# Performance work log

Measured on AMD Instinct MI355X. Metric: run time of the kernel, lower is better.

Reference implementation:

```python
import jax, jax.numpy as jnp
import numpy as np

N = 100000   # nodes
E = 1600000  # edges
D = 128      # input_dim == hidden_dim
G = 64       # graphs in batch
EPS = 1e-5


def setup_inputs() -> dict:
    key = jax.random.key(0)
    ks = jax.random.split(key, 16)
    s = 1.0 / np.sqrt(D)
    inp = {
        "x": jax.random.normal(ks[0], (N, D), jnp.float32),
        "edge_index": jax.random.randint(ks[1], (2, E), 0, N, jnp.int64),
        "batch": jnp.sort(jax.random.randint(ks[2], (N,), 0, G, jnp.int64)),
        # 4 blocks x 2 SAGEConv layers = 8 convs, all DxD
        "Wl": jax.random.normal(ks[3], (8, D, D), jnp.float32) * s,
        "bl": jnp.zeros((8, D), jnp.float32),
        "Wr": jax.random.normal(ks[4], (8, D, D), jnp.float32) * s,
        "gamma": jnp.ones((4, D), jnp.float32),
        "beta": jnp.zeros((4, D), jnp.float32),
        # classifier: 2D -> D -> D//2 -> 1
        "W1": jax.random.normal(ks[5], (2 * D, D), jnp.float32) / np.sqrt(2 * D),
        "b1": jnp.zeros((D,), jnp.float32),
        "W2": jax.random.normal(ks[6], (D, D // 2), jnp.float32) * s,
        "b2": jnp.zeros((D // 2,), jnp.float32),
        "W3": jax.random.normal(ks[7], (D // 2, 1), jnp.float32) / np.sqrt(D // 2),
        "b3": jnp.zeros((1,), jnp.float32),
    }
    return inp


def _sage_conv(h, src, dst, inv_deg, W_l, b_l, W_r):
    # mean-aggregate neighbor features (messages flow src -> dst)
    agg = jax.ops.segment_sum(h[src], dst, num_segments=N) * inv_deg
    return agg @ W_l + b_l + h @ W_r


def _forward(x, edge_index, batch, Wl, bl, Wr, gamma, beta, W1, b1, W2, b2, W3, b3):
    src, dst = edge_index[0], edge_index[1]
    deg = jax.ops.segment_sum(jnp.ones((E,), x.dtype), dst, num_segments=N)
    inv_deg = (1.0 / jnp.maximum(deg, 1.0))[:, None]  # [N,1]

    h = x
    for blk in range(4):
        # GraphSAGE(in, hid, num_layers=2): conv -> relu -> conv
        h = _sage_conv(h, src, dst, inv_deg, Wl[2 * blk], bl[2 * blk], Wr[2 * blk])
        h = jax.nn.relu(h)
        h = _sage_conv(h, src, dst, inv_deg, Wl[2 * blk + 1], bl[2 * blk + 1], Wr[2 * blk + 1])
        # BatchNorm1d over nodes (training-mode batch statistics, biased var)
        mu = jnp.mean(h, axis=0)
        var = jnp.var(h, axis=0)
        h = (h - mu) * jax.lax.rsqrt(var + EPS) * gamma[blk] + beta[blk]
        h = jax.nn.relu(h)  # dropout is identity in eval mode

    # global mean / max pool over graph ids
    cnt = jax.ops.segment_sum(jnp.ones((N,), h.dtype), batch, num_segments=G)
    x_mean = jax.ops.segment_sum(h, batch, num_segments=G) / jnp.maximum(cnt, 1.0)[:, None]
    x_max = jax.ops.segment_max(h, batch, num_segments=G)
    g = jnp.concatenate([x_mean, x_max], axis=1)  # [G, 2D]

    g = jax.nn.relu(g @ W1 + b1)
    g = jax.nn.relu(g @ W2 + b2)
    return g @ W3 + b3  # [G, 1]


def reference(x, edge_index, batch, Wl, bl, Wr, gamma, beta, W1, b1, W2, b2, W3, b3):
    return _forward(x, edge_index, batch, Wl, bl, Wr, gamma, beta, W1, b1, W2, b2, W3, b3)
```

## Files before the change

### kernel.cpp

```cpp
#include <hip/hip_runtime.h>
#include <hip/hip_bf16.h>
#include <math.h>

#define NN 100000
#define NE 1600000
#define DIM 128
#define NG 64
#define EPSBN 1e-5f
#define NGB 1563
#define SORT_WIN 12500
#define NBINBLK 6250
#define DSL 64

typedef unsigned int u32;
typedef unsigned short u16;
typedef __attribute__((ext_vector_type(8))) short bf8_t;
typedef __attribute__((ext_vector_type(4))) float f4_t;
typedef __attribute__((ext_vector_type(4))) unsigned short u16x4;
#define MFMA(a, b, c) __builtin_amdgcn_mfma_f32_16x16x32_bf16((a), (b), (c), 0, 0, 0)

__device__ __forceinline__ u16 f2bf(float f) {
    u32 u = __float_as_uint(f);
    u32 r = u + 0x7FFFu + ((u >> 16) & 1u);
    return (u16)(r >> 16);
}
__device__ __forceinline__ float bf2f(u16 h) { return __uint_as_float(((u32)h) << 16); }

__global__ void k_bin_cnt(const int* __restrict__ ei, int* __restrict__ blkcnt) {
    __shared__ int c[8];
    int t = threadIdx.x;
    if (t < 8) c[t] = 0;
    __syncthreads();
    int e = blockIdx.x * 256 + t;
    int d = ei[NE + e];
    atomicAdd(&c[d / SORT_WIN], 1);
    __syncthreads();
    if (t < 8) blkcnt[blockIdx.x * 8 + t] = c[t];
}

__global__ void k_bin_scan(const int* __restrict__ blkcnt, int* __restrict__ blkoff,
                           int* __restrict__ wtotal) {
    __shared__ int ps[256];
    int w = blockIdx.x, t = threadIdx.x;
    const int PER = (NBINBLK + 255) / 256;
    int s = 0;
    for (int i = 0; i < PER; ++i) {
        int b = t * PER + i;
        if (b < NBINBLK) s += blkcnt[b * 8 + w];
    }
    ps[t] = s;
    for (int off = 1; off < 256; off <<= 1) {
        __syncthreads();
        int x = (t >= off) ? ps[t - off] : 0;
        __syncthreads();
        ps[t] += x;
    }
    __syncthreads();
    int run = (t ? ps[t - 1] : 0);
    for (int i = 0; i < PER; ++i) {
        int b = t * PER + i;
        if (b < NBINBLK) { blkoff[b * 8 + w] = run; run += blkcnt[b * 8 + w]; }
    }
    if (t == 255) wtotal[w] = ps[255];
}

__global__ void k_bin_start(const int* __restrict__ wtotal, int* __restrict__ binStart) {
    if (threadIdx.x == 0) {
        int a = 0;
        for (int w = 0; w < 8; ++w) { binStart[w] = a; a += wtotal[w]; }
        binStart[8] = a;
    }
}

__global__ void k_bin_place(const int* __restrict__ ei, const int* __restrict__ blkoff,
                            const int* __restrict__ binStart, int2* __restrict__ binned) {
    __shared__ int base[8];
    int t = threadIdx.x;
    if (t < 8) base[t] = binStart[t] + blkoff[blockIdx.x * 8 + t];
    __syncthreads();
    int e = blockIdx.x * 256 + t;
    int s = ei[e], d = ei[NE + e];
    int pos = atomicAdd(&base[d / SORT_WIN], 1);
    binned[pos] = make_int2(s, d);
}

__global__ void k_deg2(const int2* __restrict__ binned, const int* __restrict__ binStart,
                       int* __restrict__ deg) {
    int w = blockIdx.x & 7, sl = blockIdx.x >> 3;
    int b0 = binStart[w], b1 = binStart[w + 1];
    int chunk = (b1 - b0 + DSL - 1) / DSL;
    int r0 = b0 + sl * chunk, r1 = min(r0 + chunk, b1);
    for (int i = r0 + threadIdx.x; i < r1; i += 256)
        atomicAdd(&deg[binned[i].y], 1);
}

__global__ void k_scatter(const int2* __restrict__ binned, const int* __restrict__ binStart,
                          int* __restrict__ cursor, int* __restrict__ sorted_src) {
    int w = blockIdx.x & 7, sl = blockIdx.x >> 3;
    int b0 = binStart[w], b1 = binStart[w + 1];
    int chunk = (b1 - b0 + DSL - 1) / DSL;
    int r0 = b0 + sl * chunk, r1 = min(r0 + chunk, b1);
    for (int i = r0 + threadIdx.x; i < r1; i += 256) {
        int2 e = binned[i];
        int pos = atomicAdd(&cursor[e.y], 1);
        sorted_src[pos] = e.x;
    }
}

#define SCAN_B 256
__global__ void k_scan1(const int* __restrict__ deg, int* __restrict__ row_start,
                        int* __restrict__ bsum, float* __restrict__ inv_deg) {
    __shared__ int s[SCAN_B];
    int t = threadIdx.x;
    int i = blockIdx.x * SCAN_B + t;
    int v = (i < NN) ? deg[i] : 0;
    if (i < NN) inv_deg[i] = 1.0f / (float)(v > 1 ? v : 1);
    s[t] = v;
    for (int off = 1; off < SCAN_B; off <<= 1) {
        __syncthreads();
        int x = (t >= off) ? s[t - off] : 0;
        __syncthreads();
        s[t] += x;
    }
    if (i < NN) row_start[i + 1] = s[t];
    if (t == SCAN_B - 1) bsum[blockIdx.x] = s[t];
}

__global__ void k_scan2(int* __restrict__ bsum, int nb) {
    __shared__ int s[512];
    int t = threadIdx.x;
    int v = (t < nb) ? bsum[t] : 0;
    s[t] = v;
    for (int off = 1; off < 512; off <<= 1) {
        __syncthreads();
        int x = (t >= off) ? s[t - off] : 0;
        __syncthreads();
        s[t] += x;
    }
    if (t < nb) bsum[t] = s[t] - v;
}

__global__ void k_scan3(int* __restrict__ row_start, const int* __restrict__ bsum,
                        int* __restrict__ cursor) {
    int i = blockIdx.x * blockDim.x + threadIdx.x;
    if (i < NN) {
        int v = row_start[i + 1] + bsum[i / SCAN_B];
        row_start[i + 1] = v;
        if (i + 1 < NN) cursor[i + 1] = v;
    }
    if (i == 0) { row_start[0] = 0; cursor[0] = 0; }
}

__global__ void k_bounds(const int* __restrict__ batch, int* __restrict__ gs) {
    int g = threadIdx.x;
    if (g > NG) return;
    int lo = 0, hi = NN;
    while (lo < hi) {
        int mid = (lo + hi) >> 1;
        if (batch[mid] < g) lo = mid + 1; else hi = mid;
    }
    gs[g] = lo;
}

__global__ void k_split_x(const float* __restrict__ x, u16* __restrict__ Xh,
                          u16* __restrict__ Xl) {
    int idx = blockIdx.x * 256 + threadIdx.x;
    int base = idx * 4;
    float4 v = *reinterpret_cast<const float4*>(&x[base]);
    u16x4 hi, lo;
    float vv[4] = {v.x, v.y, v.z, v.w};
#pragma unroll
    for (int j = 0; j < 4; j++) {
        u16 h = f2bf(vv[j]);
        hi[j] = h;
        lo[j] = f2bf(vv[j] - bf2f(h));
    }
    *reinterpret_cast<u16x4*>(&Xh[base]) = hi;
    *reinterpret_cast<u16x4*>(&Xl[base]) = lo;
}

__global__ void k_prep_w(const float* __restrict__ Wl, const float* __restrict__ Wr,
                         u16* __restrict__ Wth, u16* __restrict__ Wtl) {
    int idx = blockIdx.x * 256 + threadIdx.x;
    int k = idx & 255;
    int col = (idx >> 8) & 127;
    int c = idx >> 15;
    float v = (k < 128) ? Wl[(c * 128 + k) * 128 + col] : Wr[(c * 128 + (k - 128)) * 128 + col];
    u16 h = f2bf(v);
    Wth[idx] = h;
    Wtl[idx] = f2bf(v - bf2f(h));
}

template <int AFF>
__global__ void k_aggregate(const u16* __restrict__ Hh,
                            const int* __restrict__ row_start, const int* __restrict__ ssrc,
                            const float* __restrict__ inv_deg, const float* __restrict__ ss,
                            u16* __restrict__ Ah, u16* __restrict__ Al) {
    int wid = blockIdx.x * 4 + (threadIdx.x >> 6);
    int lane = threadIdx.x & 63;
    int half = lane >> 5;
    int cl = lane & 31;
    if (wid >= NN) return;
    float sc0 = 0.f, sc1 = 0.f, sc2 = 0.f, sc3 = 0.f;
    float sh0 = 0.f, sh1 = 0.f, sh2 = 0.f, sh3 = 0.f;
    if (AFF) {
        float4 s4 = *reinterpret_cast<const float4*>(ss + cl * 4);
        float4 h4 = *reinterpret_cast<const float4*>(ss + 128 + cl * 4);
        sc0 = s4.x; sc1 = s4.y; sc2 = s4.z; sc3 = s4.w;
        sh0 = h4.x; sh1 = h4.y; sh2 = h4.z; sh3 = h4.w;
    }
    int beg = row_start[wid], end = row_start[wid + 1];
    int n = end - beg;
    float a0 = 0.f, a1 = 0.f, a2 = 0.f, a3 = 0.f;
#define ACCUM(vv)                                                                   \
    {                                                                               \
        float t0 = __uint_as_float((vv).x << 16);                                   \
        float t1 = __uint_as_float((vv).x & 0xFFFF0000u);                           \
        float t2 = __uint_as_float((vv).y << 16);                                   \
        float t3 = __uint_as_float((vv).y & 0xFFFF0000u);                           \
        if (AFF) {                                                                  \
            t0 = fmaxf(t0 * sc0 + sh0, 0.f); t1 = fmaxf(t1 * sc1 + sh1, 0.f);       \
            t2 = fmaxf(t2 * sc2 + sh2, 0.f); t3 = fmaxf(t3 * sc3 + sh3, 0.f);       \
        }                                                                           \
        a0 += t0; a1 += t1; a2 += t2; a3 += t3;                                     \
    }
    for (int base = 0; base < n; base += 64) {
        int rem = n - base;
        int idx = beg + base + (lane < rem ? lane : 0);
        int sv = ssrc[idx];
        int m = rem < 64 ? rem : 64;
        int j = 0;
        for (; j + 4 <= m; j += 4) {
            int sA = __shfl(sv, j + half);
            int sB = __shfl(sv, j + 2 + half);
            uint2 vA = *reinterpret_cast<const uint2*>(
                reinterpret_cast<const u32*>(Hh + (size_t)sA * DIM) + cl * 2);
            uint2 vB = *reinterpret_cast<const uint2*>(
                reinterpret_cast<const u32*>(Hh + (size_t)sB * DIM) + cl * 2);
            ACCUM(vA); ACCUM(vB);
        }
        for (; j < m; j += 2) {
            if (j + half < m) {
                int s0 = __shfl(sv, j + half);
                uint2 v = *reinterpret_cast<const uint2*>(
                    reinterpret_cast<const u32*>(Hh + (size_t)s0 * DIM) + cl * 2);
                ACCUM(v);
            }
        }
    }
#undef ACCUM
    a0 += __shfl_down(a0, 32);
    a1 += __shfl_down(a1, 32);
    a2 += __shfl_down(a2, 32);
    a3 += __shfl_down(a3, 32);
    if (half == 0) {
        float sc = inv_deg[wid];
        a0 *= sc; a1 *= sc; a2 *= sc; a3 *= sc;
        u16 h0 = f2bf(a0), h1 = f2bf(a1), h2 = f2bf(a2), h3 = f2bf(a3);
        u16 l0 = f2bf(a0 - bf2f(h0)), l1 = f2bf(a1 - bf2f(h1));
        u16 l2 = f2bf(a2 - bf2f(h2)), l3 = f2bf(a3 - bf2f(h3));
        uint2 hv = make_uint2((u32)h0 | ((u32)h1 << 16), (u32)h2 | ((u32)h3 << 16));
        uint2 lv = make_uint2((u32)l0 | ((u32)l1 << 16), (u32)l2 | ((u32)l3 << 16));
        *reinterpret_cast<uint2*>(Ah + (size_t)wid * DIM + cl * 4) = hv;
        *reinterpret_cast<uint2*>(Al + (size_t)wid * DIM + cl * 4) = lv;
    }
}

__device__ __forceinline__ void affine_split(bf8_t& h, bf8_t& l,
                                             const float* __restrict__ ss, int k0) {
#pragma unroll
    for (int j = 0; j < 8; ++j) {
        float v = bf2f((u16)h[j]) + bf2f((u16)l[j]);
        v = fmaxf(v * ss[k0 + j] + ss[128 + k0 + j], 0.f);
        u16 hh = f2bf(v);
        h[j] = (short)hh;
        l[j] = (short)f2bf(v - bf2f(hh));
    }
}

template <bool RELU, bool STATS, bool AFF2>
__global__ __launch_bounds__(256, 2) void k_gemm(
    const u16* __restrict__ A1h, const u16* __restrict__ A1l,
    const u16* __restrict__ A2h, const u16* __restrict__ A2l,
    const u16* __restrict__ Wth, const u16* __restrict__ Wtl,
    const float* __restrict__ bias, const float* __restrict__ ss,
    u16* __restrict__ Oh, u16* __restrict__ Ol,
    float* __restrict__ partials) {
    __shared__ float cs[128], cq[128];
    int t = threadIdx.x;
    int w = t >> 6, l = t & 63;
    int rl = l & 15, kg = l >> 4;
    int col0 = w * 32;
    int rbase = blockIdx.x * 64;
    int rc0 = min(rbase + rl, NN - 1);
    int rc1 = min(rbase + 16 + rl, NN - 1);
    int rc2 = min(rbase + 32 + rl, NN - 1);
    int rc3 = min(rbase + 48 + rl, NN - 1);

    bf8_t wh[2][8], wlo[2][8];
#pragma unroll
    for (int cf = 0; cf < 2; ++cf) {
        const u16* pw = Wth + (size_t)(col0 + cf * 16 + rl) * 256 + kg * 8;
        const u16* pl = Wtl + (size_t)(col0 + cf * 16 + rl) * 256 + kg * 8;
#pragma unroll
        for (int kc = 0; kc < 8; ++kc) {
            wh[cf][kc] = *reinterpret_cast<const bf8_t*>(pw + kc * 32);
            wlo[cf][kc] = *reinterpret_cast<const bf8_t*>(pl + kc * 32);
        }
    }

    f4_t acc[4][2];
#pragma unroll
    for (int i = 0; i < 4; ++i)
#pragma unroll
        for (int j = 0; j < 2; ++j) acc[i][j] = (f4_t){0.f, 0.f, 0.f, 0.f};

    bf8_t aH[4], aL[4], bH[4], bL[4];

#define LOADK(kc, H, L)                                                          \
    {                                                                            \
        const u16* _bh = ((kc) < 4) ? A1h : A2h;                                 \
        const u16* _bl = ((kc) < 4) ? A1l : A2l;                                 \
        int _ko = ((kc) & 3) * 32 + kg * 8;                                      \
        H[0] = *reinterpret_cast<const bf8_t*>(_bh + (size_t)rc0 * DIM + _ko);   \
        L[0] = *reinterpret_cast<const bf8_t*>(_bl + (size_t)rc0 * DIM + _ko);   \
        H[1] = *reinterpret_cast<const bf8_t*>(_bh + (size_t)rc1 * DIM + _ko);   \
        L[1] = *reinterpret_cast<const bf8_t*>(_bl + (size_t)rc1 * DIM + _ko);   \
        H[2] = *reinterpret_cast<const bf8_t*>(_bh + (size_t)rc2 * DIM + _ko);   \
        L[2] = *reinterpret_cast<const bf8_t*>(_bl + (size_t)rc2 * DIM + _ko);   \
        H[3] = *reinterpret_cast<const bf8_t*>(_bh + (size_t)rc3 * DIM + _ko);   \
        L[3] = *reinterpret_cast<const bf8_t*>(_bl + (size_t)rc3 * DIM + _ko);   \
    }

#define COMPK(kc, H, L)                                                          \
    {                                                                            \
        if (AFF2 && (kc) >= 4) {                                                 \
            int _k0 = ((kc) - 4) * 32 + kg * 8;                                  \
            affine_split(H[0], L[0], ss, _k0);                                   \
            affine_split(H[1], L[1], ss, _k0);                                   \
            affine_split(H[2], L[2], ss, _k0);                                   \
            affine_split(H[3], L[3], ss, _k0);                                   \
        }                                                                        \
        _Pragma("unroll")                                                        \
        for (int _rf = 0; _rf < 4; ++_rf) {                                      \
            _Pragma("unroll")                                                    \
            for (int _cf = 0; _cf < 2; ++_cf) {                                  \
                acc[_rf][_cf] = MFMA(H[_rf], wh[_cf][(kc)], acc[_rf][_cf]);      \
                acc[_rf][_cf] = MFMA(H[_rf], wlo[_cf][(kc)], acc[_rf][_cf]);     \
                acc[_rf][_cf] = MFMA(L[_rf], wh[_cf][(kc)], acc[_rf][_cf]);      \
            }                                                                    \
        }                                                                        \
    }

    LOADK(0, aH, aL)
    LOADK(1, bH, bL) COMPK(0, aH, aL)
    LOADK(2, aH, aL) COMPK(1, bH, bL)
    LOADK(3, bH, bL) COMPK(2, aH, aL)
    LOADK(4, aH, aL) COMPK(3, bH, bL)
    LOADK(5, bH, bL) COMPK(4, aH, aL)
    LOADK(6, aH, aL) COMPK(5, bH, bL)
    LOADK(7, bH, bL) COMPK(6, aH, aL)
    COMPK(7, bH, bL)
#undef LOADK
#undef COMPK

    float bv0 = bias[col0 + rl];
    float bv1 = bias[col0 + 16 + rl];
    float s0 = 0.f, q0 = 0.f, s1 = 0.f, q1 = 0.f;
#pragma unroll
    for (int rf = 0; rf < 4; ++rf) {
#pragma unroll
        for (int i = 0; i < 4; ++i) {
            int row = rbase + rf * 16 + kg * 4 + i;
            if (row < NN) {
                float v = acc[rf][0][i] + bv0;
                if (RELU) v = fmaxf(v, 0.f);
                u16 hi = f2bf(v);
                Oh[(size_t)row * DIM + col0 + rl] = hi;
                Ol[(size_t)row * DIM + col0 + rl] = f2bf(v - bf2f(hi));
                if (STATS) { s0 += v; q0 += v * v; }
                float v1 = acc[rf][1][i] + bv1;
                if (RELU) v1 = fmaxf(v1, 0.f);
                u16 hi1 = f2bf(v1);
                Oh[(size_t)row * DIM + col0 + 16 + rl] = hi1;
                Ol[(size_t)row * DIM + col0 + 16 + rl] = f2bf(v1 - bf2f(hi1));
                if (STATS) { s1 += v1; q1 += v1 * v1; }
            }
        }
    }
    if (STATS) {
        s0 += __shfl_xor(s0, 16); s0 += __shfl_xor(s0, 32);
        q0 += __shfl_xor(q0, 16); q0 += __shfl_xor(q0, 32);
        s1 += __shfl_xor(s1, 16); s1 += __shfl_xor(s1, 32);
        q1 += __shfl_xor(q1, 16); q1 += __shfl_xor(q1, 32);
        if (l < 16) {
            cs[col0 + rl] = s0; cq[col0 + rl] = q0;
            cs[col0 + 16 + rl] = s1; cq[col0 + 16 + rl] = q1;
        }
        __syncthreads();
        partials[(size_t)blockIdx.x * 256 + t] = (t < 128) ? cs[t] : cq[t - 128];
    }
}

__global__ void k_bn_r1(const float* __restrict__ partials, float* __restrict__ colpart) {
    int t = threadIdx.x;
    int b = blockIdx.x;
    int b0 = b * 49, b1 = min(b0 + 49, NGB);
    float s = 0.f;
    for (int i = b0; i < b1; ++i) s += partials[i * 256 + t];
    colpart[b * 256 + t] = s;
}

__global__ void k_bn_r2(const float* __restrict__ colpart, const float* __restrict__ gamma,
                        const float* __restrict__ beta, float* __restrict__ scaleshift) {
    __shared__ float sm[256];
    int t = threadIdx.x;
    float s = 0.f;
#pragma unroll
    for (int b = 0; b < 32; ++b) s += colpart[b * 256 + t];
    sm[t] = s;
    __syncthreads();
    if (t < 128) {
        float mu = sm[t] * (1.0f / NN);
        float var = sm[t + 128] * (1.0f / NN) - mu * mu;
        float sc = rsqrtf(var + EPSBN) * gamma[t];
        scaleshift[t] = sc;
        scaleshift[t + 128] = beta[t] - mu * sc;
    }
}

__global__ void k_pool(const u16* __restrict__ Hh, const int* __restrict__ gs,
                       const float* __restrict__ ss,
                       float* __restrict__ pSum, float* __restrict__ pMax) {
    int g = blockIdx.x >> 3, slice = blockIdx.x & 7;
    int s0 = gs[g], s1 = gs[g + 1];
    int len = s1 - s0;
    int chunk = (len + 7) >> 3;
    int r0 = s0 + slice * chunk;
    int r1 = min(r0 + chunk, s1);
    int t = threadIdx.x;
    int c2 = (t & 63) * 2, half = t >> 6;
    float sc0 = ss[c2], sc1 = ss[c2 + 1];
    float sh0 = ss[128 + c2], sh1 = ss[128 + c2 + 1];
    float sa = 0.f, sb = 0.f, ma = 0.f, mb = 0.f;
    for (int r = r0 + half; r < r1; r += 4) {
        u32 h2 = *reinterpret_cast<const u32*>(Hh + r * DIM + c2);
        float v0 = fmaxf(__uint_as_float(h2 << 16) * sc0 + sh0, 0.f);
        float v1 = fmaxf(__uint_as_float(h2 & 0xFFFF0000u) * sc1 + sh1, 0.f);
        sa += v0; sb += v1;
        ma = fmaxf(ma, v0); mb = fmaxf(mb, v1);
    }
    __shared__ float ls[4][128], lm[4][128];
    ls[half][c2] = sa; ls[half][c2 + 1] = sb;
    lm[half][c2] = ma; lm[half][c2 + 1] = mb;
    __syncthreads();
    if (t < 128) {
        float s = ls[0][t] + ls[1][t] + ls[2][t] + ls[3][t];
        float m = fmaxf(fmaxf(lm[0][t], lm[1][t]), fmaxf(lm[2][t], lm[3][t]));
        atomicAdd(&pSum[g * DIM + t], s);
        atomicMax((int*)&pMax[g * DIM + t], __float_as_int(m));
    }
}

__global__ void k_mlp(const float* __restrict__ pSum, const float* __restrict__ pMax,
                      const int* __restrict__ gs,
                      const float* __restrict__ W1, const float* __restrict__ b1,
                      const float* __restrict__ W2, const float* __restrict__ b2,
                      const float* __restrict__ W3, const float* __restrict__ b3,
                      float* __restrict__ out) {
    __shared__ float g[256], y1[128], y2[64];
    int gi = blockIdx.x;
    int t = threadIdx.x;
    int cnt = gs[gi + 1] - gs[gi];
    float inv = 1.0f / fmaxf((float)cnt, 1.0f);
    g[t] = pSum[gi * DIM + t] * inv;
    g[128 + t] = pMax[gi * DIM + t];
    __syncthreads();
    float a = b1[t];
    for (int k = 0; k < 256; k++) a += g[k] * W1[k * 128 + t];
    y1[t] = fmaxf(a, 0.f);
    __syncthreads();
    if (t < 64) {
        float a2 = b2[t];
        for (int k = 0; k < 128; k++) a2 += y1[k] * W2[k * 64 + t];
        y2[t] = fmaxf(a2, 0.f);
    }
    __syncthreads();
    if (t < 64) {
        float p = y2[t] * W3[t];
#pragma unroll
        for (int off = 32; off; off >>= 1) p += __shfl_down(p, off);
        if (t == 0) out[gi] = p + b3[0];
    }
}

extern "C" void kernel_launch(void* const* d_in, const int* in_sizes, int n_in,
                              void* d_out, int out_size, void* d_ws, size_t ws_size,
                              hipStream_t stream) {
    const float* x     = (const float*)d_in[0];
    const int*   ei    = (const int*)d_in[1];
    const int*   batch = (const int*)d_in[2];
    const float* Wl    = (const float*)d_in[3];
    const float* bl    = (const float*)d_in[4];
    const float* Wr    = (const float*)d_in[5];
    const float* gamma = (const float*)d_in[6];
    const float* beta  = (const float*)d_in[7];
    const float* W1    = (const float*)d_in[8];
    const float* b1    = (const float*)d_in[9];
    const float* W2    = (const float*)d_in[10];
    const float* b2    = (const float*)d_in[11];
    const float* W3    = (const float*)d_in[12];
    const float* b3    = (const float*)d_in[13];
    float* out = (float*)d_out;

    char* p = (char*)d_ws;
    size_t off = 0;
    auto alloc = [&](size_t bytes) -> void* {
        void* r = p + off;
        off += (bytes + 255) & ~(size_t)255;
        return r;
    };
    const size_t HB = (size_t)NN * DIM * 2;
    u16* Xh   = (u16*)alloc(HB);
    u16* Xl   = (u16*)alloc(HB);
    u16* hAh  = (u16*)alloc(HB);
    u16* hAl  = (u16*)alloc(HB);
    u16* aggh = (u16*)alloc(HB);
    u16* aggl = (u16*)alloc(HB);
    int*   ssrc      = (int*)alloc((size_t)NE * 4);
    u16*   Wth       = (u16*)alloc((size_t)8 * 128 * 256 * 2);
    u16*   Wtl       = (u16*)alloc((size_t)8 * 128 * 256 * 2);
    float* partials  = (float*)alloc((size_t)NGB * 256 * 4);
    float* colpart   = (float*)alloc(32 * 256 * 4);
    int*   deg       = (int*)alloc(NN * 4);
    float* inv_deg   = (float*)alloc(NN * 4);
    int*   row_start = (int*)alloc((NN + 1) * 4);
    int*   cursor    = (int*)alloc(NN * 4);
    int*   bsum      = (int*)alloc(512 * 4);
    int*   gs        = (int*)alloc((NG + 1) * 4);
    int*   blkcnt    = (int*)alloc((size_t)NBINBLK * 8 * 4);
    int*   blkoff    = (int*)alloc((size_t)NBINBLK * 8 * 4);
    int*   wtotal    = (int*)alloc(8 * 4);
    int*   binStart  = (int*)alloc(9 * 4);
    float* ssb       = (float*)alloc(4 * 256 * 4);
    float* pSum      = (float*)alloc(NG * DIM * 4);
    float* pMax      = (float*)alloc(NG * DIM * 4);
    int2*  binned    = (int2*)aggh;

    const int nbN = (NN + 255) / 256;
    const int nbQ = NN * DIM / 4 / 256;
    const int aggGrid = (NN + 3) / 4;

    hipMemsetAsync(deg, 0, NN * 4, stream);
    k_bin_cnt<<<NBINBLK, 256, 0, stream>>>(ei, blkcnt);
    k_bin_scan<<<8, 256, 0, stream>>>(blkcnt, blkoff, wtotal);
    k_bin_start<<<1, 64, 0, stream>>>(wtotal, binStart);
    k_bin_place<<<NBINBLK, 256, 0, stream>>>(ei, blkoff, binStart, binned);
    k_deg2<<<8 * DSL, 256, 0, stream>>>(binned, binStart, deg);
    k_scan1<<<nbN, 256, 0, stream>>>(deg, row_start, bsum, inv_deg);
    k_scan2<<<1, 512, 0, stream>>>(bsum, nbN);
    k_scan3<<<nbN, 256, 0, stream>>>(row_start, bsum, cursor);
    k_scatter<<<8 * DSL, 256, 0, stream>>>(binned, binStart, cursor, ssrc);
    k_bounds<<<1, 128, 0, stream>>>(batch, gs);

    k_split_x<<<nbQ, 256, 0, stream>>>(x, Xh, Xl);
    k_prep_w<<<8 * 128 * 256 / 256, 256, 0, stream>>>(Wl, Wr, Wth, Wtl);

    for (int b = 0; b < 4; b++) {
        int c0 = 2 * b, c1 = 2 * b + 1;
        const u16* W0h = Wth + (size_t)c0 * 128 * 256;
        const u16* W0l = Wtl + (size_t)c0 * 128 * 256;
        const u16* W1h = Wth + (size_t)c1 * 128 * 256;
        const u16* W1l = Wtl + (size_t)c1 * 128 * 256;
        const float* ssPrev = ssb + (size_t)(b > 0 ? b - 1 : 0) * 256;
        if (b == 0) {
            k_aggregate<0><<<aggGrid, 256, 0, stream>>>(Xh, row_start, ssrc, inv_deg,
                                                        ssPrev, aggh, aggl);
            k_gemm<true, false, false><<<NGB, 256, 0, stream>>>(
                aggh, aggl, Xh, Xl, W0h, W0l, bl + c0 * DIM, ssPrev, hAh, hAl, partials);
        } else {
            k_aggregate<1><<<aggGrid, 256, 0, stream>>>(Xh, row_start, ssrc, inv_deg,
                                                        ssPrev, aggh, aggl);
            k_gemm<true, false, true><<<NGB, 256, 0, stream>>>(
                aggh, aggl, Xh, Xl, W0h, W0l, bl + c0 * DIM, ssPrev, hAh, hAl, partials);
        }
        k_aggregate<0><<<aggGrid, 256, 0, stream>>>(hAh, row_start, ssrc, inv_deg,
                                                    ssPrev, aggh, aggl);
        k_gemm<false, true, false><<<NGB, 256, 0, stream>>>(
            aggh, aggl, hAh, hAl, W1h, W1l, bl + c1 * DIM, ssPrev, Xh, Xl, partials);
        k_bn_r1<<<32, 256, 0, stream>>>(partials, colpart);
        k_bn_r2<<<1, 256, 0, stream>>>(colpart, gamma + b * DIM, beta + b * DIM,
                                       ssb + (size_t)b * 256);
    }

    hipMemsetAsync(pSum, 0, NG * DIM * 4, stream);
    hipMemsetAsync(pMax, 0, NG * DIM * 4, stream);
    k_pool<<<NG * 8, 256, 0, stream>>>(Xh, gs, ssb + 3 * 256, pSum, pMax);
    k_mlp<<<NG, 128, 0, stream>>>(pSum, pMax, gs, W1, b1, W2, b2, W3, b3, out);
}
```

Measured before the change: 1.646 ms.

## Stage GEMM A tiles in LDS via direct global-to-LDS loads, stream weights per k

```diff
diff --git a/kernel.cpp b/kernel.cpp
--- a/kernel.cpp
+++ b/kernel.cpp
@@ -286,28 +286,32 @@
     const float* __restrict__ bias, const float* __restrict__ ss,
     u16* __restrict__ Oh, u16* __restrict__ Ol,
     float* __restrict__ partials) {
+    __shared__ u16 sA[4][64][128];
     __shared__ float cs[128], cq[128];
     int t = threadIdx.x;
     int w = t >> 6, l = t & 63;
     int rl = l & 15, kg = l >> 4;
     int col0 = w * 32;
     int rbase = blockIdx.x * 64;
-    int rc0 = min(rbase + rl, NN - 1);
-    int rc1 = min(rbase + 16 + rl, NN - 1);
-    int rc2 = min(rbase + 32 + rl, NN - 1);
-    int rc3 = min(rbase + 48 + rl, NN - 1);
-
-    bf8_t wh[2][8], wlo[2][8];
-#pragma unroll
-    for (int cf = 0; cf < 2; ++cf) {
-        const u16* pw = Wth + (size_t)(col0 + cf * 16 + rl) * 256 + kg * 8;
-        const u16* pl = Wtl + (size_t)(col0 + cf * 16 + rl) * 256 + kg * 8;
-#pragma unroll
-        for (int kc = 0; kc < 8; ++kc) {
-            wh[cf][kc] = *reinterpret_cast<const bf8_t*>(pw + kc * 32);
-            wlo[cf][kc] = *reinterpret_cast<const bf8_t*>(pl + kc * 32);
-        }
-    }
+
+    const u16* srcs[4] = {A1h, A1l, A2h, A2l};
+#pragma unroll
+    for (int R = 0; R < 4; ++R) {
+#pragma unroll
+        for (int i = 0; i < 4; ++i) {
+            int slot = i * 256 + w * 64 + l;
+            int row = slot >> 4, cm = slot & 15;
+            int cd = cm ^ (row & 7);
+            int rowc = min(rbase + row, NN - 1);
+            const u16* g = srcs[R] + (size_t)rowc * DIM + cd * 8;
+            u16* lp = &sA[R][0][0] + (size_t)(i * 256 + w * 64) * 8;
+            __builtin_amdgcn_global_load_lds(
+                (const __attribute__((address_space(1))) void*)g,
+                (__attribute__((address_space(3))) void*)lp, 16, 0, 0);
+        }
+    }
+    asm volatile("s_waitcnt vmcnt(0)" ::: "memory");
+    __syncthreads();
 
     f4_t acc[4][2];
 #pragma unroll
@@ -315,54 +319,38 @@
 #pragma unroll
         for (int j = 0; j < 2; ++j) acc[i][j] = (f4_t){0.f, 0.f, 0.f, 0.f};
 
-    bf8_t aH[4], aL[4], bH[4], bL[4];
-
-#define LOADK(kc, H, L)                                                          \
-    {                                                                            \
-        const u16* _bh = ((kc) < 4) ? A1h : A2h;                                 \
-        const u16* _bl = ((kc) < 4) ? A1l : A2l;                                 \
-        int _ko = ((kc) & 3) * 32 + kg * 8;                                      \
-        H[0] = *reinterpret_cast<const bf8_t*>(_bh + (size_t)rc0 * DIM + _ko);   \
-        L[0] = *reinterpret_cast<const bf8_t*>(_bl + (size_t)rc0 * DIM + _ko);   \
-        H[1] = *reinterpret_cast<const bf8_t*>(_bh + (size_t)rc1 * DIM + _ko);   \
-        L[1] = *reinterpret_cast<const bf8_t*>(_bl + (size_t)rc1 * DIM + _ko);   \
-        H[2] = *reinterpret_cast<const bf8_t*>(_bh + (size_t)rc2 * DIM + _ko);   \
-        L[2] = *reinterpret_cast<const bf8_t*>(_bl + (size_t)rc2 * DIM + _ko);   \
-        H[3] = *reinterpret_cast<const bf8_t*>(_bh + (size_t)rc3 * DIM + _ko);   \
-        L[3] = *reinterpret_cast<const bf8_t*>(_bl + (size_t)rc3 * DIM + _ko);   \
-    }
-
-#define COMPK(kc, H, L)                                                          \
-    {                                                                            \
-        if (AFF2 && (kc) >= 4) {                                                 \
-            int _k0 = ((kc) - 4) * 32 + kg * 8;                                  \
-            affine_split(H[0], L[0], ss, _k0);                                   \
-            affine_split(H[1], L[1], ss, _k0);                                   \
-            affine_split(H[2], L[2], ss, _k0);                                   \
-            affine_split(H[3], L[3], ss, _k0);                                   \
-        }                                                                        \
-        _Pragma("unroll")                                                        \
-        for (int _rf = 0; _rf < 4; ++_rf) {                                      \
-            _Pragma("unroll")                                                    \
-            for (int _cf = 0; _cf < 2; ++_cf) {                                  \
-                acc[_rf][_cf] = MFMA(H[_rf], wh[_cf][(kc)], acc[_rf][_cf]);      \
-                acc[_rf][_cf] = MFMA(H[_rf], wlo[_cf][(kc)], acc[_rf][_cf]);     \
-                acc[_rf][_cf] = MFMA(L[_rf], wh[_cf][(kc)], acc[_rf][_cf]);      \
-            }                                                                    \
-        }                                                                        \
-    }
-
-    LOADK(0, aH, aL)
-    LOADK(1, bH, bL) COMPK(0, aH, aL)
-    LOADK(2, aH, aL) COMPK(1, bH, bL)
-    LOADK(3, bH, bL) COMPK(2, aH, aL)
-    LOADK(4, aH, aL) COMPK(3, bH, bL)
-    LOADK(5, bH, bL) COMPK(4, aH, aL)
-    LOADK(6, aH, aL) COMPK(5, bH, bL)
-    LOADK(7, bH, bL) COMPK(6, aH, aL)
-    COMPK(7, bH, bL)
-#undef LOADK
-#undef COMPK
+#define AFRAG(R, kc, rf)                                                            \
+    (*reinterpret_cast<const bf8_t*>(                                               \
+        &sA[(R)][(rf) * 16 + rl][((((kc) & 3) * 4 + kg) ^ (rl & 7)) * 8]))
+
+#pragma unroll
+    for (int kc = 0; kc < 8; ++kc) {
+        int Rh = (kc < 4) ? 0 : 2;
+        bf8_t wh0 = *reinterpret_cast<const bf8_t*>(
+            Wth + (size_t)(col0 + rl) * 256 + kc * 32 + kg * 8);
+        bf8_t wl0 = *reinterpret_cast<const bf8_t*>(
+            Wtl + (size_t)(col0 + rl) * 256 + kc * 32 + kg * 8);
+        bf8_t wh1 = *reinterpret_cast<const bf8_t*>(
+            Wth + (size_t)(col0 + 16 + rl) * 256 + kc * 32 + kg * 8);
+        bf8_t wl1 = *reinterpret_cast<const bf8_t*>(
+            Wtl + (size_t)(col0 + 16 + rl) * 256 + kc * 32 + kg * 8);
+#pragma unroll
+        for (int rf = 0; rf < 4; ++rf) {
+            bf8_t aH = AFRAG(Rh, kc, rf);
+            bf8_t aL = AFRAG(Rh + 1, kc, rf);
+            if (AFF2 && kc >= 4) {
+                int k0 = (kc - 4) * 32 + kg * 8;
+                affine_split(aH, aL, ss, k0);
+            }
+            acc[rf][0] = MFMA(aH, wh0, acc[rf][0]);
+            acc[rf][0] = MFMA(aH, wl0, acc[rf][0]);
+            acc[rf][0] = MFMA(aL, wh0, acc[rf][0]);
+            acc[rf][1] = MFMA(aH, wh1, acc[rf][1]);
+            acc[rf][1] = MFMA(aH, wl1, acc[rf][1]);
+            acc[rf][1] = MFMA(aL, wh1, acc[rf][1]);
+        }
+    }
+#undef AFRAG
 
     float bv0 = bias[col0 + rl];
     float bv1 = bias[col0 + 16 + rl];
```

Measured after the change: 1.398 ms. 1.18x faster.
